# Kernel tuning notes

Measured on AMD Instinct MI355X. Metric: run time of the kernel, lower is better.

The kernel has to match this reference:

```python
import jax, jax.numpy as jnp
import numpy as np

T, K, D = 65536, 2048, 256


def setup_inputs() -> dict:
    key = jax.random.key(0)
    k1, k2 = jax.random.split(key)
    x_td = jax.random.normal(k1, (T, D), dtype=jnp.float32)
    # codebook initialized like build(): uniform in [-1/K, 1/K]; use normal-free uniform
    embeddings_kd = jax.random.uniform(k2, (K, D), minval=-1.0 / K, maxval=1.0 / K, dtype=jnp.float32)
    return {"x_td": x_td, "embeddings_kd": embeddings_kd}


def reference(x_td, embeddings_kd):
    x_sq_t = jnp.sum(x_td ** 2, axis=-1, keepdims=True)          # (T, 1)
    e_sq_k = jnp.sum(embeddings_kd ** 2, axis=-1)                # (K,)
    cross_tk = x_td @ embeddings_kd.T                            # (T, K)
    dist_tk = x_sq_t - 2.0 * cross_tk + e_sq_k                   # (T, K)
    indices_t = jnp.argmin(dist_tk, axis=-1)                     # (T,)
    # decode: gather codebook rows
    quantized_td = embeddings_kd[indices_t]                      # (T, D)
    # straight-through estimator
    quantized_td = x_td + jax.lax.stop_gradient(quantized_td - x_td)
    return quantized_td, indices_t
```

## Files before the change

kernel.cpp:

```cpp
#include <hip/hip_runtime.h>

#define T_SZ 65536
#define K_SZ 2048
#define D_SZ 256

typedef unsigned short u16;
typedef _Float16 f16;
typedef f16 f16x8 __attribute__((ext_vector_type(8)));
typedef float f32x4 __attribute__((ext_vector_type(4)));

#define RINGCAP 1024

__device__ __forceinline__ int swz4(int r) { return (r & 3) ^ ((r >> 2) & 3); }

__device__ __forceinline__ float pairwise128_sq_v4(const float4* __restrict__ a4) {
#pragma clang fp contract(off)
  float4 va = a4[0], vb = a4[1];
  float r0 = va.x * va.x, r1 = va.y * va.y, r2 = va.z * va.z, r3 = va.w * va.w;
  float r4 = vb.x * vb.x, r5 = vb.y * vb.y, r6 = vb.z * vb.z, r7 = vb.w * vb.w;
#pragma unroll
  for (int i = 2; i < 32; i += 2) {
    float4 c = a4[i], d = a4[i + 1];
    r0 += c.x * c.x;
    r1 += c.y * c.y;
    r2 += c.z * c.z;
    r3 += c.w * c.w;
    r4 += d.x * d.x;
    r5 += d.y * d.y;
    r6 += d.z * d.z;
    r7 += d.w * d.w;
  }
  return ((r0 + r1) + (r2 + r3)) + ((r4 + r5) + (r6 + r7));
}

__device__ __forceinline__ float2 pairwise128_sq_abs_v4(const float4* __restrict__ a4) {
#pragma clang fp contract(off)
  float4 va = a4[0], vb = a4[1];
  float r0 = va.x * va.x, r1 = va.y * va.y, r2 = va.z * va.z, r3 = va.w * va.w;
  float r4 = vb.x * vb.x, r5 = vb.y * vb.y, r6 = vb.z * vb.z, r7 = vb.w * vb.w;
  float s0 = fabsf(va.x) + fabsf(va.y), s1 = fabsf(va.z) + fabsf(va.w);
  float s2 = fabsf(vb.x) + fabsf(vb.y), s3 = fabsf(vb.z) + fabsf(vb.w);
#pragma unroll
  for (int i = 2; i < 32; i += 2) {
    float4 c = a4[i], d = a4[i + 1];
    r0 += c.x * c.x;
    r1 += c.y * c.y;
    r2 += c.z * c.z;
    r3 += c.w * c.w;
    r4 += d.x * d.x;
    r5 += d.y * d.y;
    r6 += d.z * d.z;
    r7 += d.w * d.w;
    s0 += fabsf(c.x) + fabsf(c.y);
    s1 += fabsf(c.z) + fabsf(c.w);
    s2 += fabsf(d.x) + fabsf(d.y);
    s3 += fabsf(d.z) + fabsf(d.w);
  }
  float2 res;
  res.x = ((r0 + r1) + (r2 + r3)) + ((r4 + r5) + (r6 + r7));
  res.y = (s0 + s1) + (s2 + s3);
  return res;
}

__global__ void esq_kernel(const float* __restrict__ e, float* __restrict__ esq) {
  int k = blockIdx.x * 64 + threadIdx.x;
  const float4* er = reinterpret_cast<const float4*>(e + (size_t)k * D_SZ);
  esq[k] = pairwise128_sq_v4(er) + pairwise128_sq_v4(er + 32);
}

__global__ __launch_bounds__(256) void conv_e_kernel(const float* __restrict__ src,
                                                     u16* __restrict__ dst) {
  const int tile = blockIdx.x, tid = threadIdx.x;
  const float4* s4 = reinterpret_cast<const float4*>(src);
  u16* dt = dst + (size_t)tile * 32768;
#pragma unroll 1
  for (int it = 0; it < 16; ++it) {
    int idx = tid + it * 256;
    int G = idx & 3, row = (idx >> 2) & 127, step = idx >> 9;
    int srow = tile * 128 + row;
    int kb = step * 32 + 8 * (G ^ swz4(row));
    float4 a = s4[srow * 64 + (kb >> 2)];
    float4 b = s4[srow * 64 + (kb >> 2) + 1];
    float v[8] = {a.x, a.y, a.z, a.w, b.x, b.y, b.z, b.w};
    union { f16 h[8]; uint4 vec; } pk;
#pragma unroll
    for (int j = 0; j < 8; ++j) pk.h[j] = (f16)v[j];
    *reinterpret_cast<uint4*>(dt + (size_t)step * 4096 + row * 32 + G * 8) = pk.vec;
  }
}

__device__ __forceinline__ float exact_cross(const float4* __restrict__ x4,
                                             const float4* __restrict__ e4,
                                             int grow, int code) {
  const float4* xr = x4 + (size_t)grow * 64;
  const float4* er = e4 + (size_t)code * 64;
  float acc = 0.0f;
#pragma unroll 8
  for (int t = 0; t < 64; ++t) {
    float4 a = xr[t], b = er[t];
    acc = __builtin_fmaf(a.x, b.x, acc);
    acc = __builtin_fmaf(a.y, b.y, acc);
    acc = __builtin_fmaf(a.z, b.z, acc);
    acc = __builtin_fmaf(a.w, b.w, acc);
  }
  return acc;
}

__global__ __launch_bounds__(256, 4) void vq_mfma_kernel(
    const float* __restrict__ x, const float* __restrict__ e,
    const u16* __restrict__ Eh, const float* __restrict__ esq_g,
    float* __restrict__ out, float* __restrict__ outIdx) {
  __shared__ __align__(16) u16 As[8][64][32];
  __shared__ float xsq_s[64], th_s[64];
  __shared__ unsigned rm1_u[64];
  __shared__ unsigned ring[RINGCAP];
  __shared__ unsigned long long ebest[64];
  __shared__ int fidx[64];
  __shared__ unsigned ringcnt;

  const int tid = threadIdx.x;
  const int lane = tid & 63;
  const int wm = (tid >> 6) >> 1, wn = (tid >> 6) & 1;
  const int rowbase = blockIdx.x * 64;

  if (tid == 0) ringcnt = 0;
  if (tid < 64) {
    ebest[tid] = ~0ull;
    rm1_u[tid] = 0x7F7FFFFFu;
  }

  const float4* x4 = reinterpret_cast<const float4*>(x);

  const float4* xt4 = x4 + (size_t)rowbase * 64;
#pragma unroll 2
  for (int it = 0; it < 8; ++it) {
    int idx = tid + it * 256;
    int G = idx & 3, row = (idx >> 2) & 63, ks = idx >> 8;
    int kb = ks * 32 + 8 * (G ^ swz4(row));
    float4 a = xt4[(size_t)row * 64 + (kb >> 2)];
    float4 b = xt4[(size_t)row * 64 + (kb >> 2) + 1];
    union { f16 h[8]; uint4 vec; } pk;
    pk.h[0] = (f16)a.x; pk.h[1] = (f16)a.y; pk.h[2] = (f16)a.z; pk.h[3] = (f16)a.w;
    pk.h[4] = (f16)b.x; pk.h[5] = (f16)b.y; pk.h[6] = (f16)b.z; pk.h[7] = (f16)b.w;
    *reinterpret_cast<uint4*>(&As[ks][row][G * 8]) = pk.vec;
  }

  if (tid < 64) {
    const float4* xr = x4 + (size_t)(rowbase + tid) * 64;
    float2 p0 = pairwise128_sq_abs_v4(xr);
    float2 p1 = pairwise128_sq_abs_v4(xr + 32);
    xsq_s[tid] = p0.x + p1.x;
    th_s[tid] = 4.0e-6f * (p0.y + p1.y) + 4.0e-4f;
  }

  int offA[2], offB[4];
#pragma unroll
  for (int mf = 0; mf < 2; ++mf) {
    const int row = wm * 32 + mf * 16 + (lane & 15);
    offA[mf] = row * 32 + (((lane >> 4) ^ swz4(row)) * 8);
  }
#pragma unroll
  for (int nf = 0; nf < 4; ++nf) {
    const int cl = wn * 64 + nf * 16 + (lane & 15);
    offB[nf] = cl * 32 + (((lane >> 4) ^ swz4(cl)) * 8);
  }

  f32x4 acc[2][4];
#pragma unroll
  for (int mf = 0; mf < 2; ++mf)
#pragma unroll
    for (int nf = 0; nf < 4; ++nf) acc[mf][nf] = (f32x4){0.f, 0.f, 0.f, 0.f};

  f16x8 bpf[2][4];
#pragma unroll
  for (int nf = 0; nf < 4; ++nf)
    bpf[0][nf] = *reinterpret_cast<const f16x8*>(Eh + offB[nf]);

  __syncthreads();

#pragma unroll 1
  for (int chunk = 0; chunk < 16; ++chunk) {
    float esq_c[4];
#pragma unroll
    for (int nf = 0; nf < 4; ++nf)
      esq_c[nf] = esq_g[chunk * 128 + wn * 64 + nf * 16 + (lane & 15)];
#pragma unroll
    for (int ks = 0; ks < 8; ++ks) {
      const int par = ks & 1;
      const int gsn = chunk * 8 + ks + 1;
      if (gsn < 128) {
        const u16* bg = Eh + (size_t)gsn * 4096;
#pragma unroll
        for (int nf = 0; nf < 4; ++nf)
          bpf[par ^ 1][nf] = *reinterpret_cast<const f16x8*>(bg + offB[nf]);
      }
      const u16* aa = &As[ks][0][0];
      f16x8 afr[2];
#pragma unroll
      for (int mf = 0; mf < 2; ++mf)
        afr[mf] = *reinterpret_cast<const f16x8*>(aa + offA[mf]);
#pragma unroll
      for (int mf = 0; mf < 2; ++mf)
#pragma unroll
        for (int nf = 0; nf < 4; ++nf)
          acc[mf][nf] = __builtin_amdgcn_mfma_f32_16x16x32_f16(
              afr[mf], bpf[par][nf], acc[mf][nf], 0, 0, 0);
    }
#pragma unroll
    for (int mf = 0; mf < 2; ++mf) {
#pragma unroll
      for (int rg = 0; rg < 4; ++rg) {
        const int row = wm * 32 + mf * 16 + (lane >> 4) * 4 + rg;
        const float xq = xsq_s[row];
        float dmin = 3.4e38f;
#pragma unroll
        for (int nf = 0; nf < 4; ++nf)
          dmin = fminf(dmin, (xq - 2.0f * acc[mf][nf][rg]) + esq_c[nf]);
        dmin = fminf(dmin, __shfl_xor(dmin, 1, 64));
        dmin = fminf(dmin, __shfl_xor(dmin, 2, 64));
        dmin = fminf(dmin, __shfl_xor(dmin, 4, 64));
        dmin = fminf(dmin, __shfl_xor(dmin, 8, 64));
        if ((lane & 15) == 0) atomicMin(&rm1_u[row], __float_as_uint(dmin));
      }
    }
    __syncthreads();
    const int cbase = chunk * 128 + wn * 64;
#pragma unroll
    for (int mf = 0; mf < 2; ++mf) {
#pragma unroll
      for (int rg = 0; rg < 4; ++rg) {
        const int row = wm * 32 + mf * 16 + (lane >> 4) * 4 + rg;
        const float xq = xsq_s[row];
        const float gate = __uint_as_float(rm1_u[row]) + th_s[row];
#pragma unroll
        for (int nf = 0; nf < 4; ++nf) {
          const float dv = (xq - 2.0f * acc[mf][nf][rg]) + esq_c[nf];
          if (dv <= gate) {
            unsigned slot = atomicAdd(&ringcnt, 1u);
            if (slot < RINGCAP)
              ring[slot] = ((unsigned)row << 11) |
                           (unsigned)(cbase + nf * 16 + (lane & 15));
          }
          acc[mf][nf][rg] = 0.0f;
        }
      }
    }
  }
  __syncthreads();

  const float4* e4 = reinterpret_cast<const float4*>(e);
  const unsigned cnt = ringcnt;
  if (cnt <= RINGCAP) {
    for (unsigned i = tid; i < cnt; i += 256) {
      const unsigned ent = ring[i];
      const int row = (int)(ent >> 11), code = (int)(ent & 2047u);
      const float cr = exact_cross(x4, e4, rowbase + row, code);
      const float d = (xsq_s[row] - 2.0f * cr) + esq_g[code];
      const unsigned long long key =
          (((unsigned long long)__float_as_uint(d)) << 32) | (unsigned)code;
      atomicMin(&ebest[row], key);
    }
  } else {
#pragma unroll 1
    for (int row = 0; row < 64; ++row) {
      for (int code = tid; code < K_SZ; code += 256) {
        const float cr = exact_cross(x4, e4, rowbase + row, code);
        const float d = (xsq_s[row] - 2.0f * cr) + esq_g[code];
        const unsigned long long key =
            (((unsigned long long)__float_as_uint(d)) << 32) | (unsigned)code;
        atomicMin(&ebest[row], key);
      }
    }
  }
  __syncthreads();
  if (tid < 64) fidx[tid] = (int)(ebest[tid] & 2047ull);
  __syncthreads();

  float4* out4 = reinterpret_cast<float4*>(out);
#pragma unroll 1
  for (int i = tid; i < 64 * 64; i += 256) {
    const int row = i >> 6, q = i & 63;
    const int idx = fidx[row];
    float4 xv = x4[(size_t)(rowbase + row) * 64 + q];
    float4 qv = e4[(size_t)idx * 64 + q];
    float4 o;
    o.x = xv.x + (qv.x - xv.x);
    o.y = xv.y + (qv.y - xv.y);
    o.z = xv.z + (qv.z - xv.z);
    o.w = xv.w + (qv.w - xv.w);
    out4[(size_t)(rowbase + row) * 64 + q] = o;
    if (q == 0) outIdx[rowbase + row] = (float)idx;
  }
}

extern "C" void kernel_launch(void* const* d_in, const int* in_sizes, int n_in,
                              void* d_out, int out_size, void* d_ws, size_t ws_size,
                              hipStream_t stream) {
  const float* x = (const float*)d_in[0];
  const float* e = (const float*)d_in[1];
  float* out = (float*)d_out;
  float* outIdx = out + (size_t)T_SZ * D_SZ;

  float* esq = (float*)d_ws;
  u16* Eh = (u16*)(esq + K_SZ);

  conv_e_kernel<<<K_SZ / 128, 256, 0, stream>>>(e, Eh);
  esq_kernel<<<K_SZ / 64, 64, 0, stream>>>(e, esq);
  vq_mfma_kernel<<<T_SZ / 64, 256, 0, stream>>>(x, e, Eh, esq, out, outIdx);
}
```

Baseline: 324.3 us.

## Keep x tile fragments in registers instead of LDS, retune waves per EU

The fp16-converted x tile now lives in registers for the whole kernel instead of being staged in shared memory, so the LDS reads inside the inner MFMA loop go away and the kernel's LDS footprint shrinks. Each lane loads its own A fragments straight from global memory with the matching k layout. To make room for the 16 extra f16x8 registers per lane, the launch bounds switch from min 4 blocks to amdgpu_waves_per_eu(3,3), which lowers occupancy in exchange for register space. The risk is register pressure and less latency hiding.

```diff
diff --git a/kernel.cpp b/kernel.cpp
--- a/kernel.cpp
+++ b/kernel.cpp
@@ -106,11 +106,11 @@
   return acc;
 }
 
-__global__ __launch_bounds__(256, 4) void vq_mfma_kernel(
+__global__ __launch_bounds__(256)
+__attribute__((amdgpu_waves_per_eu(3, 3))) void vq_mfma_kernel(
     const float* __restrict__ x, const float* __restrict__ e,
     const u16* __restrict__ Eh, const float* __restrict__ esq_g,
     float* __restrict__ out, float* __restrict__ outIdx) {
-  __shared__ __align__(16) u16 As[8][64][32];
   __shared__ float xsq_s[64], th_s[64];
   __shared__ unsigned rm1_u[64];
   __shared__ unsigned ring[RINGCAP];
@@ -131,18 +131,32 @@
 
   const float4* x4 = reinterpret_cast<const float4*>(x);
 
-  const float4* xt4 = x4 + (size_t)rowbase * 64;
-#pragma unroll 2
-  for (int it = 0; it < 8; ++it) {
-    int idx = tid + it * 256;
-    int G = idx & 3, row = (idx >> 2) & 63, ks = idx >> 8;
-    int kb = ks * 32 + 8 * (G ^ swz4(row));
-    float4 a = xt4[(size_t)row * 64 + (kb >> 2)];
-    float4 b = xt4[(size_t)row * 64 + (kb >> 2) + 1];
-    union { f16 h[8]; uint4 vec; } pk;
-    pk.h[0] = (f16)a.x; pk.h[1] = (f16)a.y; pk.h[2] = (f16)a.z; pk.h[3] = (f16)a.w;
-    pk.h[4] = (f16)b.x; pk.h[5] = (f16)b.y; pk.h[6] = (f16)b.z; pk.h[7] = (f16)b.w;
-    *reinterpret_cast<uint4*>(&As[ks][row][G * 8]) = pk.vec;
+  int offB[4];
+#pragma unroll
+  for (int nf = 0; nf < 4; ++nf) {
+    const int cl = wn * 64 + nf * 16 + (lane & 15);
+    offB[nf] = cl * 32 + (((lane >> 4) ^ swz4(cl)) * 8);
+  }
+
+  f16x8 bpf[2][4];
+#pragma unroll
+  for (int nf = 0; nf < 4; ++nf)
+    bpf[0][nf] = *reinterpret_cast<const f16x8*>(Eh + offB[nf]);
+
+  f16x8 af[2][8];
+#pragma unroll
+  for (int mf = 0; mf < 2; ++mf) {
+    const int rowA = rowbase + wm * 32 + mf * 16 + (lane & 15);
+    const size_t base = (size_t)rowA * 64 + (lane >> 4) * 2;
+#pragma unroll
+    for (int ks = 0; ks < 8; ++ks) {
+      float4 a = x4[base + ks * 8];
+      float4 b = x4[base + ks * 8 + 1];
+      f16x8 t;
+      t[0] = (f16)a.x; t[1] = (f16)a.y; t[2] = (f16)a.z; t[3] = (f16)a.w;
+      t[4] = (f16)b.x; t[5] = (f16)b.y; t[6] = (f16)b.z; t[7] = (f16)b.w;
+      af[mf][ks] = t;
+    }
   }
 
   if (tid < 64) {
@@ -153,28 +167,11 @@
     th_s[tid] = 4.0e-6f * (p0.y + p1.y) + 4.0e-4f;
   }
 
-  int offA[2], offB[4];
-#pragma unroll
-  for (int mf = 0; mf < 2; ++mf) {
-    const int row = wm * 32 + mf * 16 + (lane & 15);
-    offA[mf] = row * 32 + (((lane >> 4) ^ swz4(row)) * 8);
-  }
-#pragma unroll
-  for (int nf = 0; nf < 4; ++nf) {
-    const int cl = wn * 64 + nf * 16 + (lane & 15);
-    offB[nf] = cl * 32 + (((lane >> 4) ^ swz4(cl)) * 8);
-  }
-
   f32x4 acc[2][4];
 #pragma unroll
   for (int mf = 0; mf < 2; ++mf)
 #pragma unroll
     for (int nf = 0; nf < 4; ++nf) acc[mf][nf] = (f32x4){0.f, 0.f, 0.f, 0.f};
-
-  f16x8 bpf[2][4];
-#pragma unroll
-  for (int nf = 0; nf < 4; ++nf)
-    bpf[0][nf] = *reinterpret_cast<const f16x8*>(Eh + offB[nf]);
 
   __syncthreads();
 
@@ -194,17 +191,12 @@
         for (int nf = 0; nf < 4; ++nf)
           bpf[par ^ 1][nf] = *reinterpret_cast<const f16x8*>(bg + offB[nf]);
       }
-      const u16* aa = &As[ks][0][0];
-      f16x8 afr[2];
-#pragma unroll
-      for (int mf = 0; mf < 2; ++mf)
-        afr[mf] = *reinterpret_cast<const f16x8*>(aa + offA[mf]);
 #pragma unroll
       for (int mf = 0; mf < 2; ++mf)
 #pragma unroll
         for (int nf = 0; nf < 4; ++nf)
           acc[mf][nf] = __builtin_amdgcn_mfma_f32_16x16x32_f16(
-              afr[mf], bpf[par][nf], acc[mf][nf], 0, 0, 0);
+              af[mf][ks], bpf[par][nf], acc[mf][nf], 0, 0, 0);
     }
 #pragma unroll
     for (int mf = 0; mf < 2; ++mf) {
```

Measured after the change: 411.9 us. +27.0%, slower.
